# Kernel optimization log

Hardware: AMD Instinct MI355X
Metric: run time of the kernel (lower is better)

Reference implementation:

```python
import jax, jax.numpy as jnp
import numpy as np

ESP = 1e-10  # matches SRKNN.ESP
K = 16       # top-k neighbors


def _logmap(x):
    # sign-preserving log map (repo helper not shown; eps matches SRKNN.ESP)
    return jnp.sign(x) * jnp.log(jnp.abs(x) + ESP)


def setup_inputs() -> dict:
    key = jax.random.key(0)
    k1, k2, k3, k4 = jax.random.split(key, 4)
    B, C, H, W = 2, 128, 32, 32
    C2 = C // 2
    X = jax.random.normal(k1, (B, C, H, W), jnp.float32)
    # nn.Linear(C, C//2, bias=False) weights, torch layout [out, in]
    W_min = jax.random.normal(k2, (C2, C), jnp.float32) * 0.08
    W_sub = jax.random.normal(k3, (C2, C), jnp.float32) * 0.08
    M = jax.random.normal(k4, (C2, C2), jnp.float32)
    return {"X": X, "W_min": W_min, "W_sub": W_sub, "M": M}


def reference(X, W_min, W_sub, M):
    B, C, H, W = X.shape
    XV = jnp.transpose(X, (0, 2, 3, 1)).reshape(B, -1, C)  # [B, N, C]
    N = XV.shape[1]
    # project then log-map; pairwise (i=minuend, j=subtrahend) without repeat
    pm = _logmap(XV @ W_min.T)  # [B, N, C2]
    ps = _logmap(XV @ W_sub.T)  # [B, N, C2]
    subR = jax.nn.sigmoid(pm[:, :, None, :] - ps[:, None, :, :])  # [B, N, N, C2]
    A = M.T @ M  # [C2, C2] learned Mahalanobis metric
    dis = jnp.sqrt(jnp.sum(jnp.einsum('bijc,cd->bijd', subR, A) * subR, axis=-1))  # [B,N,N]
    diff = jax.nn.sigmoid(-dis)
    value, index = jax.lax.top_k(diff, K)  # [B, N, K]
    value = -value.reshape(B, -1, 1)       # [B, N*K, 1]
    index = index.reshape(B, -1)           # [B, N*K]
    return index, value
```

## Files before the change

kernel.cpp:

```cpp
#include <hip/hip_runtime.h>
#include <hip/hip_bf16.h>
#include <math.h>

#define NN 1024
#define CC 128
#define C2 64
#define KK 16
#define NCAND 20

#if __has_builtin(__builtin_amdgcn_exp2f)
#define EXP2F(x) __builtin_amdgcn_exp2f(x)
#else
#define EXP2F(x) exp2f(x)
#endif
#define LOG2E 1.4426950408889634f

typedef short short8 __attribute__((ext_vector_type(8)));
typedef float f32x4  __attribute__((ext_vector_type(4)));
typedef int   int4v  __attribute__((ext_vector_type(4)));
typedef unsigned int uint;

__device__ __forceinline__ float fast_rcp(float x) {
    return __builtin_amdgcn_rcpf(x);
}
__device__ __forceinline__ unsigned short f2bf(float x) {
    unsigned int u = __float_as_uint(x);
    unsigned int r = (u + 0x7FFFu + ((u >> 16) & 1u)) >> 16;
    return (unsigned short)r;
}
__device__ __forceinline__ float bf2f(unsigned short h) {
    return __uint_as_float(((unsigned int)h) << 16);
}

#define LDS_FENCE() do { \
    asm volatile("s_waitcnt lgkmcnt(0)" ::: "memory"); \
    __builtin_amdgcn_sched_barrier(0); } while (0)

__global__ __launch_bounds__(256) void buildA(const float* __restrict__ M,
                                              float* __restrict__ A) {
    const int e = blockIdx.x * 256 + threadIdx.x;
    const int c = e >> 6, d = e & 63;
    float acc = 0.f;
    #pragma unroll 8
    for (int r = 0; r < C2; ++r)
        acc = fmaf(M[r * C2 + c], M[r * C2 + d], acc);
    A[e] = acc;
}

__global__ __launch_bounds__(128) void proj(
        const float* __restrict__ X,
        const float* __restrict__ Wm,
        const float* __restrict__ Ws,
        float* __restrict__ pm,
        float* __restrict__ ps,
        float* __restrict__ psE) {
    const int bn = blockIdx.x;
    const int b  = bn >> 10;
    const int n  = bn & (NN - 1);
    const int t  = threadIdx.x;

    __shared__ float xv[CC];
    xv[t] = X[b * CC * NN + t * NN + n];
    __syncthreads();

    const int d = t & (C2 - 1);
    const float* wr = ((t < C2) ? Wm : Ws) + d * CC;
    float acc = 0.f;
    #pragma unroll
    for (int c = 0; c < CC; ++c)
        acc = fmaf(wr[c], xv[c], acc);

    float a = __fadd_rn(fabsf(acc), 1e-10f);
    float l = logf(a);
    float r = (acc > 0.f) ? l : ((acc < 0.f) ? -l : 0.f);
    if (t < C2) {
        pm[bn * C2 + d] = r;
    } else {
        ps[bn * C2 + d] = r;
        psE[bn * C2 + d] = EXP2F(r * LOG2E);
    }
}

#define SIG_PACK(PMEF, Y0, Y1, KT, BHI, BLO) do {                             \
    float s0 = PMEF[KT][0] * fast_rcp(PMEF[KT][0] + (Y0).x);                  \
    float s1 = PMEF[KT][1] * fast_rcp(PMEF[KT][1] + (Y0).y);                  \
    float s2 = PMEF[KT][2] * fast_rcp(PMEF[KT][2] + (Y0).z);                  \
    float s3 = PMEF[KT][3] * fast_rcp(PMEF[KT][3] + (Y0).w);                  \
    float s4 = PMEF[KT][4] * fast_rcp(PMEF[KT][4] + (Y1).x);                  \
    float s5 = PMEF[KT][5] * fast_rcp(PMEF[KT][5] + (Y1).y);                  \
    float s6 = PMEF[KT][6] * fast_rcp(PMEF[KT][6] + (Y1).z);                  \
    float s7 = PMEF[KT][7] * fast_rcp(PMEF[KT][7] + (Y1).w);                  \
    uint u0 = __float_as_uint(s0), u1 = __float_as_uint(s1);                  \
    uint u2 = __float_as_uint(s2), u3 = __float_as_uint(s3);                  \
    uint u4 = __float_as_uint(s4), u5 = __float_as_uint(s5);                  \
    uint u6 = __float_as_uint(s6), u7 = __float_as_uint(s7);                  \
    uint l0 = __float_as_uint(s0 - __uint_as_float(u0 & 0xFFFF0000u));        \
    uint l1 = __float_as_uint(s1 - __uint_as_float(u1 & 0xFFFF0000u));        \
    uint l2 = __float_as_uint(s2 - __uint_as_float(u2 & 0xFFFF0000u));        \
    uint l3 = __float_as_uint(s3 - __uint_as_float(u3 & 0xFFFF0000u));        \
    uint l4 = __float_as_uint(s4 - __uint_as_float(u4 & 0xFFFF0000u));        \
    uint l5 = __float_as_uint(s5 - __uint_as_float(u5 & 0xFFFF0000u));        \
    uint l6 = __float_as_uint(s6 - __uint_as_float(u6 & 0xFFFF0000u));        \
    uint l7 = __float_as_uint(s7 - __uint_as_float(u7 & 0xFFFF0000u));        \
    int4v hiv = { (int)__builtin_amdgcn_perm(u1, u0, 0x07060302u),            \
                  (int)__builtin_amdgcn_perm(u3, u2, 0x07060302u),            \
                  (int)__builtin_amdgcn_perm(u5, u4, 0x07060302u),            \
                  (int)__builtin_amdgcn_perm(u7, u6, 0x07060302u) };          \
    int4v lov = { (int)__builtin_amdgcn_perm(l1, l0, 0x07060302u),            \
                  (int)__builtin_amdgcn_perm(l3, l2, 0x07060302u),            \
                  (int)__builtin_amdgcn_perm(l5, l4, 0x07060302u),            \
                  (int)__builtin_amdgcn_perm(l7, l6, 0x07060302u) };          \
    BHI = __builtin_bit_cast(short8, hiv);                                    \
    BLO = __builtin_bit_cast(short8, lov);                                    \
} while (0)

#define MFMA12(AC, KT, BHI, BLO)                                                        \
    AC[0] = __builtin_amdgcn_mfma_f32_16x16x32_bf16(ahi[0][KT], BHI, AC[0], 0, 0, 0);   \
    AC[0] = __builtin_amdgcn_mfma_f32_16x16x32_bf16(ahi[0][KT], BLO, AC[0], 0, 0, 0);   \
    AC[0] = __builtin_amdgcn_mfma_f32_16x16x32_bf16(alo[0][KT], BHI, AC[0], 0, 0, 0);   \
    AC[1] = __builtin_amdgcn_mfma_f32_16x16x32_bf16(ahi[1][KT], BHI, AC[1], 0, 0, 0);   \
    AC[1] = __builtin_amdgcn_mfma_f32_16x16x32_bf16(ahi[1][KT], BLO, AC[1], 0, 0, 0);   \
    AC[1] = __builtin_amdgcn_mfma_f32_16x16x32_bf16(alo[1][KT], BHI, AC[1], 0, 0, 0);   \
    AC[2] = __builtin_amdgcn_mfma_f32_16x16x32_bf16(ahi[2][KT], BHI, AC[2], 0, 0, 0);   \
    AC[2] = __builtin_amdgcn_mfma_f32_16x16x32_bf16(ahi[2][KT], BLO, AC[2], 0, 0, 0);   \
    AC[2] = __builtin_amdgcn_mfma_f32_16x16x32_bf16(alo[2][KT], BHI, AC[2], 0, 0, 0);   \
    AC[3] = __builtin_amdgcn_mfma_f32_16x16x32_bf16(ahi[3][KT], BHI, AC[3], 0, 0, 0);   \
    AC[3] = __builtin_amdgcn_mfma_f32_16x16x32_bf16(ahi[3][KT], BLO, AC[3], 0, 0, 0);   \
    AC[3] = __builtin_amdgcn_mfma_f32_16x16x32_bf16(alo[3][KT], BHI, AC[3], 0, 0, 0);

#define STREAM(PMEF, T0, T1, T2, T3, AC) do {                                 \
    short8 bh0, bl0, bh1, bl1;                                                \
    SIG_PACK(PMEF, T0, T1, 0, bh0, bl0);                                      \
    SIG_PACK(PMEF, T2, T3, 1, bh1, bl1);                                      \
    MFMA12(AC, 0, bh0, bl0)                                                   \
    MFMA12(AC, 1, bh1, bl1)                                                   \
} while (0)

__global__ __launch_bounds__(256, 2) void pair_topk(
        const float* __restrict__ pm,
        const float* __restrict__ ps,
        const float* __restrict__ psE,
        const float* __restrict__ Mf,
        const float* __restrict__ A,
        float* __restrict__ out) {
    const int tid  = threadIdx.x;
    const int wv   = tid >> 6;
    const int lane = tid & 63;
    const int g    = lane >> 4;
    const int lj   = lane & 15;
    const int rp   = wv >> 1;
    const int h    = wv & 1;

    const int rbase = blockIdx.x * 4;
    const int b     = rbase >> 10;

    __shared__ uint  d2u[4][NN];
    __shared__ float sC[4][C2];
    __shared__ float cdiffL[4][NCAND];

    const float* psb  = ps  + b * NN * C2;
    const float* psEb = psE + b * NN * C2;

    {
        const int r0 = rbase + rp * 2;

        float pmEf0[2][8], pmEf1[2][8];
        #pragma unroll
        for (int kt = 0; kt < 2; ++kt) {
            const float4 a0 = *(const float4*)(pm + r0 * C2 + kt * 32 + g * 8);
            const float4 a1 = *(const float4*)(pm + r0 * C2 + kt * 32 + g * 8 + 4);
            pmEf0[kt][0] = EXP2F(a0.x * LOG2E); pmEf0[kt][1] = EXP2F(a0.y * LOG2E);
            pmEf0[kt][2] = EXP2F(a0.z * LOG2E); pmEf0[kt][3] = EXP2F(a0.w * LOG2E);
            pmEf0[kt][4] = EXP2F(a1.x * LOG2E); pmEf0[kt][5] = EXP2F(a1.y * LOG2E);
            pmEf0[kt][6] = EXP2F(a1.z * LOG2E); pmEf0[kt][7] = EXP2F(a1.w * LOG2E);
            const float4 c0 = *(const float4*)(pm + (r0 + 1) * C2 + kt * 32 + g * 8);
            const float4 c1 = *(const float4*)(pm + (r0 + 1) * C2 + kt * 32 + g * 8 + 4);
            pmEf1[kt][0] = EXP2F(c0.x * LOG2E); pmEf1[kt][1] = EXP2F(c0.y * LOG2E);
            pmEf1[kt][2] = EXP2F(c0.z * LOG2E); pmEf1[kt][3] = EXP2F(c0.w * LOG2E);
            pmEf1[kt][4] = EXP2F(c1.x * LOG2E); pmEf1[kt][5] = EXP2F(c1.y * LOG2E);
            pmEf1[kt][6] = EXP2F(c1.z * LOG2E); pmEf1[kt][7] = EXP2F(c1.w * LOG2E);
        }

        short8 ahi[4][2], alo[4][2];
        #pragma unroll
        for (int rt = 0; rt < 4; ++rt) {
            #pragma unroll
            for (int kt = 0; kt < 2; ++kt) {
                const float* mrow = Mf + (rt * 16 + lj) * C2 + kt * 32 + g * 8;
                const float4 m0 = *(const float4*)mrow;
                const float4 m1 = *(const float4*)(mrow + 4);
                float mv[8] = {m0.x, m0.y, m0.z, m0.w, m1.x, m1.y, m1.z, m1.w};
                #pragma unroll
                for (int e = 0; e < 8; ++e) {
                    unsigned short hh = f2bf(mv[e]);
                    ahi[rt][kt][e] = (short)hh;
                    alo[rt][kt][e] = (short)f2bf(mv[e] - bf2f(hh));
                }
            }
        }

        const int tbase = h * 32;
        const float* p0 = psEb + (long)((tbase + 0) * 16 + lj) * C2 + g * 8;
        const float* p1 = psEb + (long)((tbase + 1) * 16 + lj) * C2 + g * 8;
        float4 cA0 = *(const float4*)(p0);      float4 cA1 = *(const float4*)(p0 + 4);
        float4 cA2 = *(const float4*)(p0 + 32); float4 cA3 = *(const float4*)(p0 + 36);
        float4 cB0 = *(const float4*)(p1);      float4 cB1 = *(const float4*)(p1 + 4);
        float4 cB2 = *(const float4*)(p1 + 32); float4 cB3 = *(const float4*)(p1 + 36);

        #pragma unroll 1
        for (int it = 0; it < 16; ++it) {
            float4 nA0, nA1, nA2, nA3, nB0, nB1, nB2, nB3;
            if (it < 15) {
                const float* q0 = psEb + (long)((tbase + it * 2 + 2) * 16 + lj) * C2 + g * 8;
                const float* q1 = psEb + (long)((tbase + it * 2 + 3) * 16 + lj) * C2 + g * 8;
                nA0 = *(const float4*)(q0);      nA1 = *(const float4*)(q0 + 4);
                nA2 = *(const float4*)(q0 + 32); nA3 = *(const float4*)(q0 + 36);
                nB0 = *(const float4*)(q1);      nB1 = *(const float4*)(q1 + 4);
                nB2 = *(const float4*)(q1 + 32); nB3 = *(const float4*)(q1 + 36);
            }

            f32x4 a0A[4] = {{0,0,0,0},{0,0,0,0},{0,0,0,0},{0,0,0,0}};
            f32x4 a1A[4] = {{0,0,0,0},{0,0,0,0},{0,0,0,0},{0,0,0,0}};
            f32x4 a0B[4] = {{0,0,0,0},{0,0,0,0},{0,0,0,0},{0,0,0,0}};
            f32x4 a1B[4] = {{0,0,0,0},{0,0,0,0},{0,0,0,0},{0,0,0,0}};

            __builtin_amdgcn_s_setprio(1);
            STREAM(pmEf0, cA0, cA1, cA2, cA3, a0A);
            STREAM(pmEf1, cA0, cA1, cA2, cA3, a1A);
            STREAM(pmEf0, cB0, cB1, cB2, cB3, a0B);
            STREAM(pmEf1, cB0, cB1, cB2, cB3, a1B);
            __builtin_amdgcn_s_setprio(0);

            float s0A = 0.f, s1A = 0.f, s0B = 0.f, s1B = 0.f;
            #pragma unroll
            for (int e = 0; e < 4; ++e) {
                s0A = fmaf(a0A[0][e], a0A[0][e], s0A);
                s0A = fmaf(a0A[1][e], a0A[1][e], s0A);
                s0A = fmaf(a0A[2][e], a0A[2][e], s0A);
                s0A = fmaf(a0A[3][e], a0A[3][e], s0A);
                s1A = fmaf(a1A[0][e], a1A[0][e], s1A);
                s1A = fmaf(a1A[1][e], a1A[1][e], s1A);
                s1A = fmaf(a1A[2][e], a1A[2][e], s1A);
                s1A = fmaf(a1A[3][e], a1A[3][e], s1A);
                s0B = fmaf(a0B[0][e], a0B[0][e], s0B);
                s0B = fmaf(a0B[1][e], a0B[1][e], s0B);
                s0B = fmaf(a0B[2][e], a0B[2][e], s0B);
                s0B = fmaf(a0B[3][e], a0B[3][e], s0B);
                s1B = fmaf(a1B[0][e], a1B[0][e], s1B);
                s1B = fmaf(a1B[1][e], a1B[1][e], s1B);
                s1B = fmaf(a1B[2][e], a1B[2][e], s1B);
                s1B = fmaf(a1B[3][e], a1B[3][e], s1B);
            }
            s0A += __shfl_xor(s0A, 16, 64); s0A += __shfl_xor(s0A, 32, 64);
            s1A += __shfl_xor(s1A, 16, 64); s1A += __shfl_xor(s1A, 32, 64);
            s0B += __shfl_xor(s0B, 16, 64); s0B += __shfl_xor(s0B, 32, 64);
            s1B += __shfl_xor(s1B, 16, 64); s1B += __shfl_xor(s1B, 32, 64);
            if (lane < 16) {
                const int jA = (tbase + it * 2 + 0) * 16 + lane;
                const int jB = (tbase + it * 2 + 1) * 16 + lane;
                d2u[rp * 2 + 0][jA] = (__float_as_uint(s0A) & 0xFFFFFC00u) | (uint)jA;
                d2u[rp * 2 + 1][jA] = (__float_as_uint(s1A) & 0xFFFFFC00u) | (uint)jA;
                d2u[rp * 2 + 0][jB] = (__float_as_uint(s0B) & 0xFFFFFC00u) | (uint)jB;
                d2u[rp * 2 + 1][jB] = (__float_as_uint(s1B) & 0xFFFFFC00u) | (uint)jB;
            }

            cA0 = nA0; cA1 = nA1; cA2 = nA2; cA3 = nA3;
            cB0 = nB0; cB1 = nB1; cB2 = nB2; cB3 = nB3;
        }
    }
    __syncthreads();

    const int bi = rbase + wv;
    const int i  = bi & (NN - 1);
    const float pm_own = pm[bi * C2 + lane];

    uint v[16];
    #pragma unroll
    for (int q = 0; q < 16; ++q) v[q] = d2u[wv][q * 64 + lane];

    int myCand = 0;
    #pragma unroll 1
    for (int k = 0; k < NCAND; ++k) {
        uint bv = v[0];
        #pragma unroll
        for (int q = 1; q < 16; ++q) bv = min(bv, v[q]);
        #pragma unroll
        for (int st = 0; st < 6; ++st)
            bv = min(bv, (uint)__shfl_xor((int)bv, 1 << st, 64));
        #pragma unroll
        for (int q = 0; q < 16; ++q)
            if (v[q] == bv) v[q] = 0xFFFFFFFFu;
        if (lane == k) myCand = (int)(bv & 0x3FFu);
    }

    float Acol[C2];
    #pragma unroll
    for (int c = 0; c < C2; ++c) Acol[c] = A[c * C2 + lane];

    int jvv[NCAND];
    #pragma unroll
    for (int t = 0; t < NCAND; ++t) jvv[t] = __shfl(myCand, t, 64);
    float pscv[NCAND];
    #pragma unroll
    for (int t = 0; t < NCAND; ++t) pscv[t] = psb[(long)jvv[t] * C2 + lane];

    #pragma unroll 1
    for (int t = 0; t < NCAND; ++t) {
        float e = expf(pscv[t] - pm_own);
        float s_own = 1.0f / __fadd_rn(1.0f, e);
        sC[wv][lane] = s_own;
        LDS_FENCE();
        float wd = 0.f;
        #pragma unroll
        for (int c = 0; c < C2; ++c)
            wd = fmaf(sC[wv][c], Acol[c], wd);
        const float t_own = __fmul_rn(wd, s_own);
        float r8 = t_own;
        #pragma unroll
        for (int blk = 1; blk < 8; ++blk)
            r8 = __fadd_rn(r8, __shfl(t_own, (lane & 7) + 8 * blk, 64));
        const float rr0 = __shfl(r8, 0, 64), rr1 = __shfl(r8, 1, 64);
        const float rr2 = __shfl(r8, 2, 64), rr3 = __shfl(r8, 3, 64);
        const float rr4 = __shfl(r8, 4, 64), rr5 = __shfl(r8, 5, 64);
        const float rr6 = __shfl(r8, 6, 64), rr7 = __shfl(r8, 7, 64);
        float dis2 = __fadd_rn(
            __fadd_rn(__fadd_rn(rr0, rr1), __fadd_rn(rr2, rr3)),
            __fadd_rn(__fadd_rn(rr4, rr5), __fadd_rn(rr6, rr7)));
        float disf = sqrtf(dis2);
        float ee = expf(disf);
        float cd = 1.0f / __fadd_rn(1.0f, ee);
        if (lane == 0) cdiffL[wv][t] = cd;
    }
    LDS_FENCE();

    float myd = (lane < NCAND) ? cdiffL[wv][lane] : -2.0f;
    int myj = (lane < NCAND) ? myCand : (1 << 20);

    const int obase = b * (NN * KK) + i * KK;
    const int vbase = 2 * NN * KK + obase;

    #pragma unroll 1
    for (int k = 0; k < KK; ++k) {
        float bd = myd;
        int bj = myj;
        #pragma unroll
        for (int st = 0; st < 6; ++st) {
            int msk = 1 << st;
            float od = __shfl_xor(bd, msk, 64);
            int oj = __shfl_xor(bj, msk, 64);
            bool better = (od > bd) || (od == bd && oj < bj);
            bd = better ? od : bd;
            bj = better ? oj : bj;
        }
        if (myj == bj) myd = -2.0f;
        if (lane == 0) {
            out[obase + k] = (float)bj;
            out[vbase + k] = -bd;
        }
    }
}

extern "C" void kernel_launch(void* const* d_in, const int* in_sizes, int n_in,
                              void* d_out, int out_size, void* d_ws, size_t ws_size,
                              hipStream_t stream) {
    const float* X  = (const float*)d_in[0];
    const float* Wm = (const float*)d_in[1];
    const float* Ws = (const float*)d_in[2];
    const float* M  = (const float*)d_in[3];

    float* A   = (float*)d_ws;
    float* pm  = A + C2 * C2;
    float* ps  = pm + 2 * NN * C2;
    float* psE = ps + 2 * NN * C2;
    float* out = (float*)d_out;

    hipLaunchKernelGGL(buildA, dim3(16), dim3(256), 0, stream, M, A);
    hipLaunchKernelGGL(proj, dim3(2 * NN), dim3(128), 0, stream,
                       X, Wm, Ws, pm, ps, psE);
    hipLaunchKernelGGL(pair_topk, dim3(512), dim3(256), 0, stream,
                       pm, ps, psE, M, A, out);
}
```

Before: 110.3 us.

## Switch pairwise MFMA from split-bf16 to fp16 and fuse buildA into proj

Converts the sigmoid operand to a single fp16 value packed with cvt_pkrtz instead of a hi/lo bf16 split, which cuts the MFMA count per k-tile from 12 to 8 and drops the packing arithmetic. The M matrix is still split into fp16 hi/lo parts. The buildA kernel is merged into the projection kernel as extra blocks, removing one launch. NCAND is raised to 24 to widen the candidate set, offsetting the lower precision of fp16 in the top-k selection at some extra selection cost.

```diff
diff --git a/kernel.cpp b/kernel.cpp
--- a/kernel.cpp
+++ b/kernel.cpp
@@ -1,12 +1,13 @@
 #include <hip/hip_runtime.h>
 #include <hip/hip_bf16.h>
+#include <hip/hip_fp16.h>
 #include <math.h>
 
 #define NN 1024
 #define CC 128
 #define C2 64
 #define KK 16
-#define NCAND 20
+#define NCAND 24
 
 #if __has_builtin(__builtin_amdgcn_exp2f)
 #define EXP2F(x) __builtin_amdgcn_exp2f(x)
@@ -15,45 +16,40 @@
 #endif
 #define LOG2E 1.4426950408889634f
 
-typedef short short8 __attribute__((ext_vector_type(8)));
-typedef float f32x4  __attribute__((ext_vector_type(4)));
-typedef int   int4v  __attribute__((ext_vector_type(4)));
+typedef __fp16  hf2   __attribute__((ext_vector_type(2)));
+typedef _Float16 half8 __attribute__((ext_vector_type(8)));
+typedef float f32x4    __attribute__((ext_vector_type(4)));
+typedef int   int4v    __attribute__((ext_vector_type(4)));
 typedef unsigned int uint;
 
 __device__ __forceinline__ float fast_rcp(float x) {
     return __builtin_amdgcn_rcpf(x);
 }
-__device__ __forceinline__ unsigned short f2bf(float x) {
-    unsigned int u = __float_as_uint(x);
-    unsigned int r = (u + 0x7FFFu + ((u >> 16) & 1u)) >> 16;
-    return (unsigned short)r;
-}
-__device__ __forceinline__ float bf2f(unsigned short h) {
-    return __uint_as_float(((unsigned int)h) << 16);
-}
 
 #define LDS_FENCE() do { \
     asm volatile("s_waitcnt lgkmcnt(0)" ::: "memory"); \
     __builtin_amdgcn_sched_barrier(0); } while (0)
 
-__global__ __launch_bounds__(256) void buildA(const float* __restrict__ M,
-                                              float* __restrict__ A) {
-    const int e = blockIdx.x * 256 + threadIdx.x;
-    const int c = e >> 6, d = e & 63;
-    float acc = 0.f;
-    #pragma unroll 8
-    for (int r = 0; r < C2; ++r)
-        acc = fmaf(M[r * C2 + c], M[r * C2 + d], acc);
-    A[e] = acc;
-}
-
-__global__ __launch_bounds__(128) void proj(
+__global__ __launch_bounds__(128) void proj_buildA(
         const float* __restrict__ X,
         const float* __restrict__ Wm,
         const float* __restrict__ Ws,
+        const float* __restrict__ M,
         float* __restrict__ pm,
         float* __restrict__ ps,
-        float* __restrict__ psE) {
+        float* __restrict__ psE,
+        float* __restrict__ A) {
+    if (blockIdx.x >= 2 * NN) {
+        const int e = (blockIdx.x - 2 * NN) * 128 + threadIdx.x;
+        const int c = e >> 6, d = e & 63;
+        float acc = 0.f;
+        #pragma unroll 8
+        for (int r = 0; r < C2; ++r)
+            acc = fmaf(M[r * C2 + c], M[r * C2 + d], acc);
+        A[e] = acc;
+        return;
+    }
+
     const int bn = blockIdx.x;
     const int b  = bn >> 10;
     const int n  = bn & (NN - 1);
@@ -81,59 +77,40 @@
     }
 }
 
-#define SIG_PACK(PMEF, Y0, Y1, KT, BHI, BLO) do {                             \
-    float s0 = PMEF[KT][0] * fast_rcp(PMEF[KT][0] + (Y0).x);                  \
-    float s1 = PMEF[KT][1] * fast_rcp(PMEF[KT][1] + (Y0).y);                  \
-    float s2 = PMEF[KT][2] * fast_rcp(PMEF[KT][2] + (Y0).z);                  \
-    float s3 = PMEF[KT][3] * fast_rcp(PMEF[KT][3] + (Y0).w);                  \
-    float s4 = PMEF[KT][4] * fast_rcp(PMEF[KT][4] + (Y1).x);                  \
-    float s5 = PMEF[KT][5] * fast_rcp(PMEF[KT][5] + (Y1).y);                  \
-    float s6 = PMEF[KT][6] * fast_rcp(PMEF[KT][6] + (Y1).z);                  \
-    float s7 = PMEF[KT][7] * fast_rcp(PMEF[KT][7] + (Y1).w);                  \
-    uint u0 = __float_as_uint(s0), u1 = __float_as_uint(s1);                  \
-    uint u2 = __float_as_uint(s2), u3 = __float_as_uint(s3);                  \
-    uint u4 = __float_as_uint(s4), u5 = __float_as_uint(s5);                  \
-    uint u6 = __float_as_uint(s6), u7 = __float_as_uint(s7);                  \
-    uint l0 = __float_as_uint(s0 - __uint_as_float(u0 & 0xFFFF0000u));        \
-    uint l1 = __float_as_uint(s1 - __uint_as_float(u1 & 0xFFFF0000u));        \
-    uint l2 = __float_as_uint(s2 - __uint_as_float(u2 & 0xFFFF0000u));        \
-    uint l3 = __float_as_uint(s3 - __uint_as_float(u3 & 0xFFFF0000u));        \
-    uint l4 = __float_as_uint(s4 - __uint_as_float(u4 & 0xFFFF0000u));        \
-    uint l5 = __float_as_uint(s5 - __uint_as_float(u5 & 0xFFFF0000u));        \
-    uint l6 = __float_as_uint(s6 - __uint_as_float(u6 & 0xFFFF0000u));        \
-    uint l7 = __float_as_uint(s7 - __uint_as_float(u7 & 0xFFFF0000u));        \
-    int4v hiv = { (int)__builtin_amdgcn_perm(u1, u0, 0x07060302u),            \
-                  (int)__builtin_amdgcn_perm(u3, u2, 0x07060302u),            \
-                  (int)__builtin_amdgcn_perm(u5, u4, 0x07060302u),            \
-                  (int)__builtin_amdgcn_perm(u7, u6, 0x07060302u) };          \
-    int4v lov = { (int)__builtin_amdgcn_perm(l1, l0, 0x07060302u),            \
-                  (int)__builtin_amdgcn_perm(l3, l2, 0x07060302u),            \
-                  (int)__builtin_amdgcn_perm(l5, l4, 0x07060302u),            \
-                  (int)__builtin_amdgcn_perm(l7, l6, 0x07060302u) };          \
-    BHI = __builtin_bit_cast(short8, hiv);                                    \
-    BLO = __builtin_bit_cast(short8, lov);                                    \
+#define SIGF16(PMEF, Y0, Y1, BF) do {                                         \
+    float s0 = PMEF[0] * fast_rcp(PMEF[0] + (Y0).x);                          \
+    float s1 = PMEF[1] * fast_rcp(PMEF[1] + (Y0).y);                          \
+    float s2 = PMEF[2] * fast_rcp(PMEF[2] + (Y0).z);                          \
+    float s3 = PMEF[3] * fast_rcp(PMEF[3] + (Y0).w);                          \
+    float s4 = PMEF[4] * fast_rcp(PMEF[4] + (Y1).x);                          \
+    float s5 = PMEF[5] * fast_rcp(PMEF[5] + (Y1).y);                          \
+    float s6 = PMEF[6] * fast_rcp(PMEF[6] + (Y1).z);                          \
+    float s7 = PMEF[7] * fast_rcp(PMEF[7] + (Y1).w);                          \
+    hf2 p0 = __builtin_amdgcn_cvt_pkrtz(s0, s1);                              \
+    hf2 p1 = __builtin_amdgcn_cvt_pkrtz(s2, s3);                              \
+    hf2 p2 = __builtin_amdgcn_cvt_pkrtz(s4, s5);                              \
+    hf2 p3 = __builtin_amdgcn_cvt_pkrtz(s6, s7);                              \
+    int4v iv = { __builtin_bit_cast(int, p0), __builtin_bit_cast(int, p1),    \
+                 __builtin_bit_cast(int, p2), __builtin_bit_cast(int, p3) };  \
+    BF = __builtin_bit_cast(half8, iv);                                       \
 } while (0)
 
-#define MFMA12(AC, KT, BHI, BLO)                                                        \
-    AC[0] = __builtin_amdgcn_mfma_f32_16x16x32_bf16(ahi[0][KT], BHI, AC[0], 0, 0, 0);   \
-    AC[0] = __builtin_amdgcn_mfma_f32_16x16x32_bf16(ahi[0][KT], BLO, AC[0], 0, 0, 0);   \
-    AC[0] = __builtin_amdgcn_mfma_f32_16x16x32_bf16(alo[0][KT], BHI, AC[0], 0, 0, 0);   \
-    AC[1] = __builtin_amdgcn_mfma_f32_16x16x32_bf16(ahi[1][KT], BHI, AC[1], 0, 0, 0);   \
-    AC[1] = __builtin_amdgcn_mfma_f32_16x16x32_bf16(ahi[1][KT], BLO, AC[1], 0, 0, 0);   \
-    AC[1] = __builtin_amdgcn_mfma_f32_16x16x32_bf16(alo[1][KT], BHI, AC[1], 0, 0, 0);   \
-    AC[2] = __builtin_amdgcn_mfma_f32_16x16x32_bf16(ahi[2][KT], BHI, AC[2], 0, 0, 0);   \
-    AC[2] = __builtin_amdgcn_mfma_f32_16x16x32_bf16(ahi[2][KT], BLO, AC[2], 0, 0, 0);   \
-    AC[2] = __builtin_amdgcn_mfma_f32_16x16x32_bf16(alo[2][KT], BHI, AC[2], 0, 0, 0);   \
-    AC[3] = __builtin_amdgcn_mfma_f32_16x16x32_bf16(ahi[3][KT], BHI, AC[3], 0, 0, 0);   \
-    AC[3] = __builtin_amdgcn_mfma_f32_16x16x32_bf16(ahi[3][KT], BLO, AC[3], 0, 0, 0);   \
-    AC[3] = __builtin_amdgcn_mfma_f32_16x16x32_bf16(alo[3][KT], BHI, AC[3], 0, 0, 0);
+#define MFMA8(AC, KT, B)                                                                \
+    AC[0] = __builtin_amdgcn_mfma_f32_16x16x32_f16(ahi[0][KT], B, AC[0], 0, 0, 0);      \
+    AC[0] = __builtin_amdgcn_mfma_f32_16x16x32_f16(alo[0][KT], B, AC[0], 0, 0, 0);      \
+    AC[1] = __builtin_amdgcn_mfma_f32_16x16x32_f16(ahi[1][KT], B, AC[1], 0, 0, 0);      \
+    AC[1] = __builtin_amdgcn_mfma_f32_16x16x32_f16(alo[1][KT], B, AC[1], 0, 0, 0);      \
+    AC[2] = __builtin_amdgcn_mfma_f32_16x16x32_f16(ahi[2][KT], B, AC[2], 0, 0, 0);      \
+    AC[2] = __builtin_amdgcn_mfma_f32_16x16x32_f16(alo[2][KT], B, AC[2], 0, 0, 0);      \
+    AC[3] = __builtin_amdgcn_mfma_f32_16x16x32_f16(ahi[3][KT], B, AC[3], 0, 0, 0);      \
+    AC[3] = __builtin_amdgcn_mfma_f32_16x16x32_f16(alo[3][KT], B, AC[3], 0, 0, 0);
 
 #define STREAM(PMEF, T0, T1, T2, T3, AC) do {                                 \
-    short8 bh0, bl0, bh1, bl1;                                                \
-    SIG_PACK(PMEF, T0, T1, 0, bh0, bl0);                                      \
-    SIG_PACK(PMEF, T2, T3, 1, bh1, bl1);                                      \
-    MFMA12(AC, 0, bh0, bl0)                                                   \
-    MFMA12(AC, 1, bh1, bl1)                                                   \
+    half8 b0, b1;                                                             \
+    SIGF16(PMEF[0], T0, T1, b0);                                              \
+    SIGF16(PMEF[1], T2, T3, b1);                                              \
+    MFMA8(AC, 0, b0)                                                          \
+    MFMA8(AC, 1, b1)                                                          \
 } while (0)
 
 __global__ __launch_bounds__(256, 2) void pair_topk(
@@ -181,7 +158,7 @@
             pmEf1[kt][6] = EXP2F(c1.z * LOG2E); pmEf1[kt][7] = EXP2F(c1.w * LOG2E);
         }
 
-        short8 ahi[4][2], alo[4][2];
+        half8 ahi[4][2], alo[4][2];
         #pragma unroll
         for (int rt = 0; rt < 4; ++rt) {
             #pragma unroll
@@ -192,9 +169,9 @@
                 float mv[8] = {m0.x, m0.y, m0.z, m0.w, m1.x, m1.y, m1.z, m1.w};
                 #pragma unroll
                 for (int e = 0; e < 8; ++e) {
-                    unsigned short hh = f2bf(mv[e]);
-                    ahi[rt][kt][e] = (short)hh;
-                    alo[rt][kt][e] = (short)f2bf(mv[e] - bf2f(hh));
+                    _Float16 hh = (_Float16)mv[e];
+                    ahi[rt][kt][e] = hh;
+                    alo[rt][kt][e] = (_Float16)(mv[e] - (float)hh);
                 }
             }
         }
@@ -374,9 +351,8 @@
     float* psE = ps + 2 * NN * C2;
     float* out = (float*)d_out;
 
-    hipLaunchKernelGGL(buildA, dim3(16), dim3(256), 0, stream, M, A);
-    hipLaunchKernelGGL(proj, dim3(2 * NN), dim3(128), 0, stream,
-                       X, Wm, Ws, pm, ps, psE);
+    hipLaunchKernelGGL(proj_buildA, dim3(2 * NN + 32), dim3(128), 0, stream,
+                       X, Wm, Ws, M, pm, ps, psE, A);
     hipLaunchKernelGGL(pair_topk, dim3(512), dim3(256), 0, stream,
                        pm, ps, psE, M, A, out);
 }
```

New measurement: 98.86 us. 1.12x faster.
